# Optimization experiments

Measured on AMD Instinct MI355X. Metric: run time of the kernel, lower is better.

Reference implementation:

```python
import jax, jax.numpy as jnp
import numpy as np

N, E, D, H, C, ED = 50000, 800000, 128, 4, 32, 1
EFF = H * C  # 128 == D, so residual proj is Identity
FFN_H = 2 * EFF


def setup_inputs() -> dict:
    key = jax.random.key(0)
    ks = jax.random.split(key, 16)
    def p(k, shape, fan_in):
        return jax.random.normal(k, shape, dtype=jnp.float32) / np.sqrt(fan_in)
    return {
        "x": jax.random.normal(ks[0], (N, D), dtype=jnp.float32),
        "edge_attr": jax.random.normal(ks[1], (E, ED), dtype=jnp.float32),
        "W_l": p(ks[2], (D, EFF), D),
        "b_l": jnp.zeros((EFF,), jnp.float32),
        "W_r": p(ks[3], (D, EFF), D),
        "b_r": jnp.zeros((EFF,), jnp.float32),
        "W_e": p(ks[4], (ED, EFF), ED),
        "att": p(ks[5], (H, C), C),
        "bias_out": jnp.zeros((EFF,), jnp.float32),
        "W_gate": p(ks[6], (EFF, 1), EFF),
        "b_gate": jnp.zeros((1,), jnp.float32),
        "W_ffn1": p(ks[7], (EFF, FFN_H), EFF),
        "b_ffn1": jnp.zeros((FFN_H,), jnp.float32),
        "W_ffn2": p(ks[8], (FFN_H, EFF), FFN_H),
        "b_ffn2": jnp.zeros((EFF,), jnp.float32),
        "ln_gamma": jnp.ones((EFF,), jnp.float32),
        "ln_beta": jnp.zeros((EFF,), jnp.float32),
        "edge_index": jax.random.randint(ks[9], (2, E), 0, N, dtype=jnp.int32),
    }


def _gat_block(x, edge_attr, W_l, b_l, W_r, b_r, W_e, att, bias_out,
               W_gate, b_gate, W_ffn1, b_ffn1, W_ffn2, b_ffn2,
               ln_gamma, ln_beta, edge_index):
    n = x.shape[0]
    # add self loops (PyG default), edge_attr filled with mean
    loop = jnp.arange(n, dtype=edge_index.dtype)
    src = jnp.concatenate([edge_index[0], loop])
    dst = jnp.concatenate([edge_index[1], loop])
    ea = jnp.concatenate([edge_attr,
                          jnp.broadcast_to(edge_attr.mean(0, keepdims=True), (n, edge_attr.shape[1]))])
    # GATv2: separate source/target transforms + edge embedding
    xl = (x @ W_l + b_l).reshape(n, H, C)   # source features
    xr = (x @ W_r + b_r).reshape(n, H, C)   # target features
    ee = (ea @ W_e).reshape(-1, H, C)
    xj = xl[src]                             # [Et,H,C]
    m = jax.nn.leaky_relu(xj + xr[dst] + ee, negative_slope=0.2)
    logits = jnp.einsum('ehc,hc->eh', m, att)           # [Et,H]
    # segment softmax over destination nodes
    mx = jax.ops.segment_max(logits, dst, num_segments=n)
    ex = jnp.exp(logits - mx[dst])
    den = jax.ops.segment_sum(ex, dst, num_segments=n)
    alpha = ex / den[dst]
    out = jax.ops.segment_sum(xj * alpha[..., None], dst, num_segments=n)
    out = out.reshape(n, EFF) + bias_out
    # block: ELU, gated residual (proj is Identity since D==EFF), FFN, LayerNorm
    h = jax.nn.elu(out)
    gate = jax.nn.sigmoid(h @ W_gate + b_gate)
    y = gate * h + (1.0 - gate) * x
    ffn = jax.nn.relu(y @ W_ffn1 + b_ffn1) @ W_ffn2 + b_ffn2
    y = y + ffn
    mu = y.mean(-1, keepdims=True)
    var = y.var(-1, keepdims=True)
    y = (y - mu) * jax.lax.rsqrt(var + 1e-5) * ln_gamma + ln_beta
    return y  # dropout is identity in eval mode


def reference(x, edge_attr, W_l, b_l, W_r, b_r, W_e, att, bias_out,
              W_gate, b_gate, W_ffn1, b_ffn1, W_ffn2, b_ffn2,
              ln_gamma, ln_beta, edge_index):
    return _gat_block(x, edge_attr, W_l, b_l, W_r, b_r, W_e, att, bias_out,
                      W_gate, b_gate, W_ffn1, b_ffn1, W_ffn2, b_ffn2,
                      ln_gamma, ln_beta, edge_index)
```

## Files before the change

kernel.cpp:

```cpp
#include <hip/hip_runtime.h>
#include <hip/hip_bf16.h>

#define NODES 50000
#define NEDGE 800000
#define ETOT  850000

#define SCHUNK 1024
#define SBLK   ((NODES + SCHUNK - 1) / SCHUNK)

#define XF_TILES 1563
#define PREP_BLKS 1024
#define FUSE_GRID 2587

typedef __hip_bfloat16 bf16;
typedef __attribute__((ext_vector_type(8))) short bf16x8;
typedef __attribute__((ext_vector_type(4))) float f32x4;

__device__ __forceinline__ bf16 f2bf(float v) { return __float2bfloat16(v); }
__device__ __forceinline__ float bflo(unsigned int v) { return __uint_as_float(v << 16); }
__device__ __forceinline__ float bfhi(unsigned int v) { return __uint_as_float(v & 0xffff0000u); }

__device__ __forceinline__ unsigned int pack2(float a, float b) {
    bf16 x = f2bf(a), y = f2bf(b);
    unsigned short xs = *reinterpret_cast<unsigned short*>(&x);
    unsigned short ys = *reinterpret_cast<unsigned short*>(&y);
    return ((unsigned int)ys << 16) | (unsigned int)xs;
}

__device__ __forceinline__ unsigned short bfbits(float v) {
    bf16 x = f2bf(v);
    return *reinterpret_cast<unsigned short*>(&x);
}

__device__ __forceinline__ void split8(const float* v, bf16x8& hi, bf16x8& lo) {
    #pragma unroll
    for (int e = 0; e < 8; ++e) {
        unsigned short hb = bfbits(v[e]);
        float hv = __uint_as_float((unsigned int)hb << 16);
        unsigned short lb = bfbits(v[e] - hv);
        ((short*)&hi)[e] = (short)hb;
        ((short*)&lo)[e] = (short)lb;
    }
}

__global__ __launch_bounds__(256) void k_wxf(const float* W_l, const float* W_r,
                                             bf16* wlh, bf16* wll,
                                             bf16* wrh, bf16* wrl) {
    int tid = blockIdx.x * blockDim.x + threadIdx.x;
    int m = tid >> 14;
    int t = tid & 16383;
    int c = t >> 7, k = t & 127;
    const float* W = m ? W_r : W_l;
    float v = W[k * 128 + c];
    unsigned short hb = bfbits(v);
    float hv = __uint_as_float((unsigned int)hb << 16);
    bf16* dh = m ? wrh : wlh;
    bf16* dl = m ? wrl : wll;
    dh[t] = f2bf(v);
    dl[t] = f2bf(v - hv);
}

__global__ __launch_bounds__(256) void k_fuse(const float* edge_attr, const int* ei,
                                              float* sum_ea, int* cnt,
                                              unsigned char* tmp_rank,
                                              const float* x,
                                              const bf16* wlh, const bf16* wll,
                                              const bf16* wrh, const bf16* wrl,
                                              const float* b_l, const float* b_r,
                                              bf16* xl, bf16* xr) {
    __shared__ __align__(16) float s_x[32][132];
    const int bid = blockIdx.x;
    int idx;
    bool isprep;
    if (bid < 2 * PREP_BLKS) { isprep = (bid & 1); idx = bid >> 1; }
    else { isprep = false; idx = PREP_BLKS + (bid - 2 * PREP_BLKS); }

    if (isprep) {
        int tid = idx * 256 + threadIdx.x;
        const int stride = PREP_BLKS * 256;
        float local = 0.f;
        for (int e = tid; e < ETOT; e += stride) {
            int dst = (e < NEDGE) ? ei[NEDGE + e] : (e - NEDGE);
            int r = atomicAdd(&cnt[dst], 1);
            tmp_rank[e] = (unsigned char)r;
            if (e < NEDGE) local += edge_attr[e];
        }
        #pragma unroll
        for (int s = 1; s < 64; s <<= 1) local += __shfl_xor(local, s, 64);
        if ((threadIdx.x & 63) == 0) atomicAdd(sum_ea, local);
        return;
    }

    const int tid = threadIdx.x;
    const int n0 = idx * 32;
    for (int it = 0; it < 4; ++it) {
        int idx4 = (it * 256 + tid) * 4;
        int n = idx4 >> 7, j = idx4 & 127;
        int node = n0 + n;
        float4 v = make_float4(0.f, 0.f, 0.f, 0.f);
        if (node < NODES) v = *(const float4*)(x + node * 128 + j);
        *(float4*)&s_x[n][j] = v;
    }
    __syncthreads();

    const int wv4  = tid >> 6;
    const int ln   = tid & 63;
    const int lrow = ln & 15;
    const int lk8  = (ln >> 4) << 3;
    const int m    = wv4 >> 1;
    const int cb   = (wv4 & 1) * 64;
    const bf16* Bh = m ? wrh : wlh;
    const bf16* Bl = m ? wrl : wll;
    const float* bias = m ? b_r : b_l;

    f32x4 acc[2][4];
    #pragma unroll
    for (int mt = 0; mt < 2; ++mt)
        #pragma unroll
        for (int i = 0; i < 4; ++i)
            acc[mt][i] = (f32x4){0.f, 0.f, 0.f, 0.f};
    #pragma unroll
    for (int kk = 0; kk < 4; ++kk) {
        int k0 = kk * 32 + lk8;
        float a0f[8], a1f[8];
        *(float4*)&a0f[0] = *(const float4*)&s_x[lrow][k0];
        *(float4*)&a0f[4] = *(const float4*)&s_x[lrow][k0 + 4];
        *(float4*)&a1f[0] = *(const float4*)&s_x[16 + lrow][k0];
        *(float4*)&a1f[4] = *(const float4*)&s_x[16 + lrow][k0 + 4];
        bf16x8 a0h, a0l, a1h, a1l;
        split8(a0f, a0h, a0l);
        split8(a1f, a1h, a1l);
        #pragma unroll
        for (int i = 0; i < 4; ++i) {
            int col = cb + (i << 4) + lrow;
            bf16x8 bh = *(const bf16x8*)(Bh + col * 128 + k0);
            bf16x8 bl = *(const bf16x8*)(Bl + col * 128 + k0);
            acc[0][i] = __builtin_amdgcn_mfma_f32_16x16x32_bf16(a0l, bh, acc[0][i], 0, 0, 0);
            acc[0][i] = __builtin_amdgcn_mfma_f32_16x16x32_bf16(a0h, bl, acc[0][i], 0, 0, 0);
            acc[0][i] = __builtin_amdgcn_mfma_f32_16x16x32_bf16(a0h, bh, acc[0][i], 0, 0, 0);
            acc[1][i] = __builtin_amdgcn_mfma_f32_16x16x32_bf16(a1l, bh, acc[1][i], 0, 0, 0);
            acc[1][i] = __builtin_amdgcn_mfma_f32_16x16x32_bf16(a1h, bl, acc[1][i], 0, 0, 0);
            acc[1][i] = __builtin_amdgcn_mfma_f32_16x16x32_bf16(a1h, bh, acc[1][i], 0, 0, 0);
        }
    }
    __syncthreads();
    bf16* s_o = (bf16*)&s_x[0][0];
    #pragma unroll
    for (int mt = 0; mt < 2; ++mt) {
        #pragma unroll
        for (int i = 0; i < 4; ++i) {
            int colg = cb + (i << 4) + lrow;
            float bv = bias[colg];
            #pragma unroll
            for (int r = 0; r < 4; ++r) {
                int row = (mt << 4) + ((ln >> 4) << 2) + r;
                s_o[row * 264 + m * 136 + colg] = f2bf(acc[mt][i][r] + bv);
            }
        }
    }
    __syncthreads();
    #pragma unroll
    for (int rep = 0; rep < 2; ++rep) {
        int idx2 = rep * 256 + tid;
        int row = idx2 >> 4, cc = (idx2 & 15) * 8;
        int node = n0 + row;
        if (node < NODES) {
            *(float4*)(xl + node * 128 + cc) = *(const float4*)(s_o + row * 264 + cc);
            *(float4*)(xr + node * 128 + cc) = *(const float4*)(s_o + row * 264 + 136 + cc);
        }
    }
}

__global__ __launch_bounds__(256) void k_scan1(const int* count, int* bsum) {
    __shared__ int s_w[4];
    const int t = threadIdx.x, b = blockIdx.x;
    const int base = b * SCHUNK + t * 4;
    int s = 0;
    #pragma unroll
    for (int e = 0; e < 4; ++e) {
        int i = base + e;
        if (i < NODES) s += count[i];
    }
    #pragma unroll
    for (int d = 1; d < 64; d <<= 1) s += __shfl_xor(s, d, 64);
    if ((t & 63) == 0) s_w[t >> 6] = s;
    __syncthreads();
    if (t == 0) bsum[b] = s_w[0] + s_w[1] + s_w[2] + s_w[3];
}

__global__ __launch_bounds__(256) void k_scan3(const int* count, const int* bsum,
                                               int* off) {
    __shared__ int s_w[4];
    __shared__ int s_base;
    const int t = threadIdx.x, b = blockIdx.x;
    const int lane = t & 63, wv = t >> 6;
    if (t < 64) {
        int v = (t < b) ? bsum[t] : 0;
        #pragma unroll
        for (int d = 1; d < 64; d <<= 1) v += __shfl_xor(v, d, 64);
        if (t == 0) s_base = v;
    }
    const int base = b * SCHUNK + t * 4;
    int v[4];
    int s = 0;
    #pragma unroll
    for (int e = 0; e < 4; ++e) {
        int i = base + e;
        v[e] = (i < NODES) ? count[i] : 0;
        s += v[e];
    }
    int inc = s;
    #pragma unroll
    for (int d = 1; d < 64; d <<= 1) {
        int y = __shfl_up(inc, d, 64);
        if (lane >= d) inc += y;
    }
    if (lane == 63) s_w[wv] = inc;
    __syncthreads();
    int woff = 0;
    #pragma unroll
    for (int w = 0; w < 4; ++w) if (w < wv) woff += s_w[w];
    int run = s_base + woff + (inc - s);
    #pragma unroll
    for (int e = 0; e < 4; ++e) {
        int i = base + e;
        if (i < NODES) {
            off[i] = run; run += v[e];
            if (i == NODES - 1) off[NODES] = run;
        }
    }
}

__global__ __launch_bounds__(256) void k_wconv(const float* W1, const float* W2,
                                               bf16* w1h, bf16* w1l,
                                               bf16* w2h, bf16* w2l) {
    int tid = blockIdx.x * blockDim.x + threadIdx.x;
    if (tid < 32768) {
        int c = tid >> 7, k = tid & 127;
        float v = W1[k * 256 + c];
        unsigned short hb = bfbits(v);
        float hv = __uint_as_float((unsigned int)hb << 16);
        w1h[tid] = f2bf(v);
        w1l[tid] = f2bf(v - hv);
    } else {
        int t = tid - 32768;
        int c = t >> 8, k = t & 255;
        float v = W2[k * 128 + c];
        unsigned short hb = bfbits(v);
        float hv = __uint_as_float((unsigned int)hb << 16);
        w2h[t] = f2bf(v);
        w2l[t] = f2bf(v - hv);
    }
}

__global__ __launch_bounds__(256) void k_place(const int* ei, const float* edge_attr,
                                               const float* sum_ea, const int* off,
                                               const unsigned char* tmp_rank,
                                               unsigned int* perm) {
    const float meanv = sum_ea[0] * (1.f / (float)NEDGE);
    int tid = blockIdx.x * blockDim.x + threadIdx.x;
    int stride = gridDim.x * blockDim.x;
    for (int e = tid; e < ETOT; e += stride) {
        int src, dst; float eav;
        if (e < NEDGE) { src = ei[e]; dst = ei[NEDGE + e]; eav = edge_attr[e]; }
        else           { src = e - NEDGE; dst = src; eav = meanv; }
        int pos = off[dst] + (int)tmp_rank[e];
        perm[pos] = ((unsigned int)bfbits(eav) << 16) | (unsigned int)src;
    }
}

__global__ __launch_bounds__(256) void k_agg(const unsigned int* xl32,
                                             const unsigned int* xr32,
                                             const unsigned int* perm, const int* off,
                                             const float* W_e, const float* att,
                                             float* outp) {
    const int lane = threadIdx.x & 63;
    const int wave0 = blockIdx.x * 4 + (threadIdx.x >> 6);
    const int nwaves = gridDim.x * 4;
    const int c = 2 * lane;
    const float we1 = W_e[c], we2 = W_e[c + 1];
    const float a1 = att[c], a2 = att[c + 1];
    for (int n = wave0; n < NODES; n += nwaves) {
        unsigned int xru = xr32[n * 64 + lane];
        float xr1 = bflo(xru), xr2 = bfhi(xru);
        int s0 = off[n], s1 = off[n + 1];
        float m = -1e30f, l = 0.f, acc1 = 0.f, acc2 = 0.f;
        int j = s0;
        for (; j + 4 <= s1; j += 4) {
            unsigned int u0 = perm[j];
            unsigned int u1 = perm[j + 1];
            unsigned int u2 = perm[j + 2];
            unsigned int u3 = perm[j + 3];
            unsigned int g0 = xl32[(u0 & 0xffffu) * 64 + lane];
            unsigned int g1 = xl32[(u1 & 0xffffu) * 64 + lane];
            unsigned int g2 = xl32[(u2 & 0xffffu) * 64 + lane];
            unsigned int g3 = xl32[(u3 & 0xffffu) * 64 + lane];
            float e0 = bfhi(u0), e1 = bfhi(u1), e2 = bfhi(u2), e3 = bfhi(u3);
            float x01 = bflo(g0), x02 = bfhi(g0);
            float x11 = bflo(g1), x12 = bfhi(g1);
            float x21 = bflo(g2), x22 = bfhi(g2);
            float x31 = bflo(g3), x32 = bfhi(g3);
            float p0, p1, p2, p3;
            {
                float v1 = x01 + xr1 + e0 * we1, v2 = x02 + xr2 + e0 * we2;
                v1 = (v1 > 0.f) ? v1 : 0.2f * v1;
                v2 = (v2 > 0.f) ? v2 : 0.2f * v2;
                p0 = v1 * a1 + v2 * a2;
            }
            {
                float v1 = x11 + xr1 + e1 * we1, v2 = x12 + xr2 + e1 * we2;
                v1 = (v1 > 0.f) ? v1 : 0.2f * v1;
                v2 = (v2 > 0.f) ? v2 : 0.2f * v2;
                p1 = v1 * a1 + v2 * a2;
            }
            {
                float v1 = x21 + xr1 + e2 * we1, v2 = x22 + xr2 + e2 * we2;
                v1 = (v1 > 0.f) ? v1 : 0.2f * v1;
                v2 = (v2 > 0.f) ? v2 : 0.2f * v2;
                p2 = v1 * a1 + v2 * a2;
            }
            {
                float v1 = x31 + xr1 + e3 * we1, v2 = x32 + xr2 + e3 * we2;
                v1 = (v1 > 0.f) ? v1 : 0.2f * v1;
                v2 = (v2 > 0.f) ? v2 : 0.2f * v2;
                p3 = v1 * a1 + v2 * a2;
            }
            p0 += __shfl_xor(p0, 1, 64); p1 += __shfl_xor(p1, 1, 64);
            p2 += __shfl_xor(p2, 1, 64); p3 += __shfl_xor(p3, 1, 64);
            p0 += __shfl_xor(p0, 2, 64); p1 += __shfl_xor(p1, 2, 64);
            p2 += __shfl_xor(p2, 2, 64); p3 += __shfl_xor(p3, 2, 64);
            p0 += __shfl_xor(p0, 4, 64); p1 += __shfl_xor(p1, 4, 64);
            p2 += __shfl_xor(p2, 4, 64); p3 += __shfl_xor(p3, 4, 64);
            p0 += __shfl_xor(p0, 8, 64); p1 += __shfl_xor(p1, 8, 64);
            p2 += __shfl_xor(p2, 8, 64); p3 += __shfl_xor(p3, 8, 64);
            float nm = fmaxf(fmaxf(m, fmaxf(p0, p1)), fmaxf(p2, p3));
            float sc = __expf(m - nm);
            float E0 = __expf(p0 - nm);
            float E1 = __expf(p1 - nm);
            float E2 = __expf(p2 - nm);
            float E3 = __expf(p3 - nm);
            l = l * sc + E0 + E1 + E2 + E3;
            acc1 = acc1 * sc + E0 * x01 + E1 * x11 + E2 * x21 + E3 * x31;
            acc2 = acc2 * sc + E0 * x02 + E1 * x12 + E2 * x22 + E3 * x32;
            m = nm;
        }
        for (; j < s1; ++j) {
            unsigned int u0 = perm[j];
            unsigned int g0 = xl32[(u0 & 0xffffu) * 64 + lane];
            float e0 = bfhi(u0);
            float x01 = bflo(g0), x02 = bfhi(g0);
            float v1 = x01 + xr1 + e0 * we1, v2 = x02 + xr2 + e0 * we2;
            v1 = (v1 > 0.f) ? v1 : 0.2f * v1;
            v2 = (v2 > 0.f) ? v2 : 0.2f * v2;
            float p = v1 * a1 + v2 * a2;
            p += __shfl_xor(p, 1, 64);
            p += __shfl_xor(p, 2, 64);
            p += __shfl_xor(p, 4, 64);
            p += __shfl_xor(p, 8, 64);
            float nm = fmaxf(m, p);
            float sc = __expf(m - nm);
            float ee = __expf(p - nm);
            l = l * sc + ee;
            acc1 = acc1 * sc + ee * x01;
            acc2 = acc2 * sc + ee * x02;
            m = nm;
        }
        float inv = 1.f / fmaxf(l, 1e-30f);
        *(float2*)(outp + n * 128 + c) = make_float2(acc1 * inv, acc2 * inv);
    }
}

__global__ __launch_bounds__(256) void k_epi(const float* out_agg, const float* x,
                                             const float* bias_out,
                                             const float* W_gate, const float* b_gate,
                                             const bf16* w1h, const bf16* w1l,
                                             const float* b_ffn1,
                                             const bf16* w2h, const bf16* w2l,
                                             const float* b_ffn2,
                                             const float* gamma, const float* beta,
                                             float* out) {
    __shared__ __align__(16) float s_y[32][132];
    __shared__ __align__(16) float s_t[32][260];
    __shared__ float s_g[32];
    __shared__ float s_mu[32], s_rs[32];
    const int tid = threadIdx.x;
    const int n0 = blockIdx.x * 32;
    int nn = NODES - n0; if (nn > 32) nn = 32;

    for (int it = 0; it < 4; ++it) {
        int idx4 = (it * 256 + tid) * 4;
        int n = idx4 >> 7, j = idx4 & 127;
        float4 w = make_float4(0.f, 0.f, 0.f, 0.f);
        if (n < nn) {
            float4 v  = *(const float4*)(out_agg + (n0 + n) * 128 + j);
            float4 bv = *(const float4*)(bias_out + j);
            float t0 = v.x + bv.x, t1 = v.y + bv.y;
            float t2 = v.z + bv.z, t3 = v.w + bv.w;
            w.x = (t0 > 0.f) ? t0 : (__expf(t0) - 1.f);
            w.y = (t1 > 0.f) ? t1 : (__expf(t1) - 1.f);
            w.z = (t2 > 0.f) ? t2 : (__expf(t2) - 1.f);
            w.w = (t3 > 0.f) ? t3 : (__expf(t3) - 1.f);
        }
        *(float4*)&s_y[n][j] = w;
    }
    __syncthreads();
    {
        int n = tid >> 3, kb = (tid & 7) * 16;
        float g = 0.f;
        #pragma unroll
        for (int k = 0; k < 16; k += 4) {
            float4 w = *(const float4*)(W_gate + kb + k);
            float4 h = *(const float4*)&s_y[n][kb + k];
            g += h.x * w.x + h.y * w.y + h.z * w.z + h.w * w.w;
        }
        g += __shfl_xor(g, 1, 64);
        g += __shfl_xor(g, 2, 64);
        g += __shfl_xor(g, 4, 64);
        if ((tid & 7) == 0) s_g[n] = 1.f / (1.f + __expf(-(g + b_gate[0])));
    }
    __syncthreads();
    for (int it = 0; it < 4; ++it) {
        int idx4 = (it * 256 + tid) * 4;
        int n = idx4 >> 7, j = idx4 & 127;
        if (n < nn) {
            float g = s_g[n];
            float4 xv = *(const float4*)(x + (n0 + n) * 128 + j);
            float4 h = *(float4*)&s_y[n][j];
            h.x = g * h.x + (1.f - g) * xv.x;
            h.y = g * h.y + (1.f - g) * xv.y;
            h.z = g * h.z + (1.f - g) * xv.z;
            h.w = g * h.w + (1.f - g) * xv.w;
            *(float4*)&s_y[n][j] = h;
        }
    }
    __syncthreads();

    const int wv   = tid >> 6;
    const int ln   = tid & 63;
    const int lrow = ln & 15;
    const int lk8  = (ln >> 4) << 3;

    f32x4 acc1[2][4];
    #pragma unroll
    for (int mt = 0; mt < 2; ++mt)
        #pragma unroll
        for (int i = 0; i < 4; ++i)
            acc1[mt][i] = (f32x4){0.f, 0.f, 0.f, 0.f};
    #pragma unroll
    for (int kk = 0; kk < 4; ++kk) {
        int k0 = kk * 32 + lk8;
        float a0f[8], a1f[8];
        *(float4*)&a0f[0] = *(const float4*)&s_y[lrow][k0];
        *(float4*)&a0f[4] = *(const float4*)&s_y[lrow][k0 + 4];
        *(float4*)&a1f[0] = *(const float4*)&s_y[16 + lrow][k0];
        *(float4*)&a1f[4] = *(const float4*)&s_y[16 + lrow][k0 + 4];
        bf16x8 a0h, a0l, a1h, a1l;
        split8(a0f, a0h, a0l);
        split8(a1f, a1h, a1l);
        #pragma unroll
        for (int i = 0; i < 4; ++i) {
            int col = (wv << 6) + (i << 4) + lrow;
            bf16x8 bh = *(const bf16x8*)(w1h + col * 128 + k0);
            bf16x8 bl = *(const bf16x8*)(w1l + col * 128 + k0);
            acc1[0][i] = __builtin_amdgcn_mfma_f32_16x16x32_bf16(a0l, bh, acc1[0][i], 0, 0, 0);
            acc1[0][i] = __builtin_amdgcn_mfma_f32_16x16x32_bf16(a0h, bl, acc1[0][i], 0, 0, 0);
            acc1[0][i] = __builtin_amdgcn_mfma_f32_16x16x32_bf16(a0h, bh, acc1[0][i], 0, 0, 0);
            acc1[1][i] = __builtin_amdgcn_mfma_f32_16x16x32_bf16(a1l, bh, acc1[1][i], 0, 0, 0);
            acc1[1][i] = __builtin_amdgcn_mfma_f32_16x16x32_bf16(a1h, bl, acc1[1][i], 0, 0, 0);
            acc1[1][i] = __builtin_amdgcn_mfma_f32_16x16x32_bf16(a1h, bh, acc1[1][i], 0, 0, 0);
        }
    }
    #pragma unroll
    for (int mt = 0; mt < 2; ++mt) {
        #pragma unroll
        for (int i = 0; i < 4; ++i) {
            int col = (wv << 6) + (i << 4) + lrow;
            float bv = b_ffn1[col];
            #pragma unroll
            for (int r = 0; r < 4; ++r) {
                int row = (mt << 4) + ((ln >> 4) << 2) + r;
                s_t[row][col] = fmaxf(acc1[mt][i][r] + bv, 0.f);
            }
        }
    }
    __syncthreads();

    f32x4 acc2[2][2];
    #pragma unroll
    for (int mt = 0; mt < 2; ++mt)
        #pragma unroll
        for (int c = 0; c < 2; ++c)
            acc2[mt][c] = (f32x4){0.f, 0.f, 0.f, 0.f};
    #pragma unroll
    for (int kk = 0; kk < 8; ++kk) {
        int k0 = kk * 32 + lk8;
        float a0f[8], a1f[8];
        *(float4*)&a0f[0] = *(const float4*)&s_t[lrow][k0];
        *(float4*)&a0f[4] = *(const float4*)&s_t[lrow][k0 + 4];
        *(float4*)&a1f[0] = *(const float4*)&s_t[16 + lrow][k0];
        *(float4*)&a1f[4] = *(const float4*)&s_t[16 + lrow][k0 + 4];
        bf16x8 a0h, a0l, a1h, a1l;
        split8(a0f, a0h, a0l);
        split8(a1f, a1h, a1l);
        #pragma unroll
        for (int c = 0; c < 2; ++c) {
            int col = (wv << 5) + (c << 4) + lrow;
            bf16x8 bh = *(const bf16x8*)(w2h + col * 256 + k0);
            bf16x8 bl = *(const bf16x8*)(w2l + col * 256 + k0);
            acc2[0][c] = __builtin_amdgcn_mfma_f32_16x16x32_bf16(a0l, bh, acc2[0][c], 0, 0, 0);
            acc2[0][c] = __builtin_amdgcn_mfma_f32_16x16x32_bf16(a0h, bl, acc2[0][c], 0, 0, 0);
            acc2[0][c] = __builtin_amdgcn_mfma_f32_16x16x32_bf16(a0h, bh, acc2[0][c], 0, 0, 0);
            acc2[1][c] = __builtin_amdgcn_mfma_f32_16x16x32_bf16(a1l, bh, acc2[1][c], 0, 0, 0);
            acc2[1][c] = __builtin_amdgcn_mfma_f32_16x16x32_bf16(a1h, bl, acc2[1][c], 0, 0, 0);
            acc2[1][c] = __builtin_amdgcn_mfma_f32_16x16x32_bf16(a1h, bh, acc2[1][c], 0, 0, 0);
        }
    }
    #pragma unroll
    for (int mt = 0; mt < 2; ++mt) {
        #pragma unroll
        for (int c = 0; c < 2; ++c) {
            int col = (wv << 5) + (c << 4) + lrow;
            float bv = b_ffn2[col];
            #pragma unroll
            for (int r = 0; r < 4; ++r) {
                int row = (mt << 4) + ((ln >> 4) << 2) + r;
                s_y[row][col] += acc2[mt][c][r] + bv;
            }
        }
    }
    __syncthreads();
    {
        int n = tid >> 3, kb = (tid & 7) * 16;
        float s = 0.f, ss = 0.f;
        #pragma unroll
        for (int k = 0; k < 16; k += 4) {
            float4 v = *(const float4*)&s_y[n][kb + k];
            s  += v.x + v.y + v.z + v.w;
            ss += v.x * v.x + v.y * v.y + v.z * v.z + v.w * v.w;
        }
        s  += __shfl_xor(s, 1, 64);  ss += __shfl_xor(ss, 1, 64);
        s  += __shfl_xor(s, 2, 64);  ss += __shfl_xor(ss, 2, 64);
        s  += __shfl_xor(s, 4, 64);  ss += __shfl_xor(ss, 4, 64);
        if ((tid & 7) == 0) {
            float mu = s * (1.f / 128.f);
            float var = ss * (1.f / 128.f) - mu * mu;
            s_mu[n] = mu;
            s_rs[n] = rsqrtf(fmaxf(var, 0.f) + 1e-5f);
        }
    }
    __syncthreads();
    for (int it = 0; it < 4; ++it) {
        int idx4 = (it * 256 + tid) * 4;
        int n = idx4 >> 7, j = idx4 & 127;
        if (n < nn) {
            float mu = s_mu[n], rs = s_rs[n];
            float4 gv = *(const float4*)(gamma + j);
            float4 bv = *(const float4*)(beta + j);
            float4 v = *(const float4*)&s_y[n][j];
            float4 o;
            o.x = (v.x - mu) * rs * gv.x + bv.x;
            o.y = (v.y - mu) * rs * gv.y + bv.y;
            o.z = (v.z - mu) * rs * gv.z + bv.z;
            o.w = (v.w - mu) * rs * gv.w + bv.w;
            *(float4*)(out + (n0 + n) * 128 + j) = o;
        }
    }
}

extern "C" void kernel_launch(void* const* d_in, const int* in_sizes, int n_in,
                              void* d_out, int out_size, void* d_ws, size_t ws_size,
                              hipStream_t stream) {
    const float* x         = (const float*)d_in[0];
    const float* edge_attr = (const float*)d_in[1];
    const int* edge_index  = (const int*)d_in[17];
    float* out = (float*)d_out;

    char* base = (char*)d_ws;
    float* sum_ea  = (float*)(base + 16);
    int*   cnt     = (int*)  (base + 32);
    int*   off     = (int*)  (base + 200032);
    unsigned int* perm = (unsigned int*)(base + 600064);
    bf16*  xl      = (bf16*) (base + 4000064);
    bf16*  xr      = (bf16*) (base + 16800064);
    int*   bsum    = (int*)  (base + 600064);
    bf16*  wxlh    = (bf16*) (base + 600064 + 1024);
    bf16*  wxll    = (bf16*) (base + 600064 + 1024 + 32768);
    bf16*  wxrh    = (bf16*) (base + 600064 + 1024 + 65536);
    bf16*  wxrl    = (bf16*) (base + 600064 + 1024 + 98304);
    bf16*  w1t_hi  = (bf16*) (base + 32);
    bf16*  w1t_lo  = (bf16*) (base + 32 + 65536);
    bf16*  w2t_hi  = (bf16*) (base + 400064);
    bf16*  w2t_lo  = (bf16*) (base + 400064 + 65536);
    unsigned char* tmp_rank = (unsigned char*)d_out;

    hipMemsetAsync(sum_ea, 0, 16, stream);
    hipMemsetAsync(cnt, 0, NODES * sizeof(int), stream);

    const int NTILES = (NODES + 31) / 32;

    k_wxf   <<<128, 256, 0, stream>>>((const float*)d_in[2], (const float*)d_in[4],
                                      wxlh, wxll, wxrh, wxrl);
    k_fuse  <<<FUSE_GRID, 256, 0, stream>>>(edge_attr, edge_index, sum_ea, cnt,
                                            tmp_rank, x,
                                            wxlh, wxll, wxrh, wxrl,
                                            (const float*)d_in[3], (const float*)d_in[5],
                                            xl, xr);
    k_scan1 <<<SBLK, 256, 0, stream>>>(cnt, bsum);
    k_scan3 <<<SBLK, 256, 0, stream>>>(cnt, bsum, off);
    k_place <<<1024, 256, 0, stream>>>(edge_index, edge_attr, sum_ea, off,
                                       tmp_rank, perm);
    k_wconv <<<256, 256, 0, stream>>>((const float*)d_in[11], (const float*)d_in[13],
                                      w1t_hi, w1t_lo, w2t_hi, w2t_lo);
    k_agg   <<<3125, 256, 0, stream>>>((const unsigned int*)xl,
                                       (const unsigned int*)xr,
                                       perm, off,
                                       (const float*)d_in[6], (const float*)d_in[7],
                                       out);
    k_epi   <<<NTILES, 256, 0, stream>>>(out, x, (const float*)d_in[8],
                                         (const float*)d_in[9], (const float*)d_in[10],
                                         w1t_hi, w1t_lo, (const float*)d_in[12],
                                         w2t_hi, w2t_lo, (const float*)d_in[14],
                                         (const float*)d_in[15], (const float*)d_in[16],
                                         out);
}
```

Baseline: 350.5 us.

## Replace global-atomic counting sort with two-level LDS radix bucketing of edges

Builds the destination-sorted CSR in two levels instead of one. First, 256 blocks each count edges per coarse 1024-node range in shared memory, and a single-block scan turns those counts into per-block offsets. Edges are then scattered into range buckets, and 49 large blocks group each range by node with LDS atomics, writing off and perm. This removes 850k global atomics on per-node counters, the byte rank buffer and the memset of the counts, at the cost of an extra pass over an 8-byte temporary, a serial scan kernel and only 49 blocks in the grouping step.

```diff
diff --git a/kernel.cpp b/kernel.cpp
--- a/kernel.cpp
+++ b/kernel.cpp
@@ -5,12 +5,13 @@
 #define NEDGE 800000
 #define ETOT  850000
 
-#define SCHUNK 1024
-#define SBLK   ((NODES + SCHUNK - 1) / SCHUNK)
+#define NRANGE 49
+#define SB 256
+#define ES ((ETOT + SB - 1) / SB)
 
 #define XF_TILES 1563
-#define PREP_BLKS 1024
-#define FUSE_GRID 2587
+#define HIST_BLKS 256
+#define FUSE_GRID (2 * HIST_BLKS + (XF_TILES - HIST_BLKS))
 
 typedef __hip_bfloat16 bf16;
 typedef __attribute__((ext_vector_type(8))) short bf16x8;
@@ -61,8 +62,7 @@
 }
 
 __global__ __launch_bounds__(256) void k_fuse(const float* edge_attr, const int* ei,
-                                              float* sum_ea, int* cnt,
-                                              unsigned char* tmp_rank,
+                                              float* sum_ea, int* rhist,
                                               const float* x,
                                               const bf16* wlh, const bf16* wll,
                                               const bf16* wrh, const bf16* wrl,
@@ -72,22 +72,27 @@
     const int bid = blockIdx.x;
     int idx;
     bool isprep;
-    if (bid < 2 * PREP_BLKS) { isprep = (bid & 1); idx = bid >> 1; }
-    else { isprep = false; idx = PREP_BLKS + (bid - 2 * PREP_BLKS); }
+    if (bid < 2 * HIST_BLKS) { isprep = (bid & 1); idx = bid >> 1; }
+    else { isprep = false; idx = HIST_BLKS + (bid - 2 * HIST_BLKS); }
 
     if (isprep) {
-        int tid = idx * 256 + threadIdx.x;
-        const int stride = PREP_BLKS * 256;
+        int* hcnt = (int*)&s_x[0][0];
+        const int t = threadIdx.x;
+        if (t < 64) hcnt[t] = 0;
+        __syncthreads();
+        const int e0 = idx * ES;
+        int e1 = e0 + ES; if (e1 > ETOT) e1 = ETOT;
         float local = 0.f;
-        for (int e = tid; e < ETOT; e += stride) {
+        for (int e = e0 + t; e < e1; e += 256) {
             int dst = (e < NEDGE) ? ei[NEDGE + e] : (e - NEDGE);
-            int r = atomicAdd(&cnt[dst], 1);
-            tmp_rank[e] = (unsigned char)r;
+            atomicAdd(&hcnt[dst >> 10], 1);
             if (e < NEDGE) local += edge_attr[e];
         }
         #pragma unroll
         for (int s = 1; s < 64; s <<= 1) local += __shfl_xor(local, s, 64);
-        if ((threadIdx.x & 63) == 0) atomicAdd(sum_ea, local);
+        if ((t & 63) == 0) atomicAdd(sum_ea, local);
+        __syncthreads();
+        if (t < 64) rhist[idx * 64 + t] = hcnt[t];
         return;
     }
 
@@ -171,63 +176,91 @@
     }
 }
 
-__global__ __launch_bounds__(256) void k_scan1(const int* count, int* bsum) {
+__global__ __launch_bounds__(256) void k_rscan(int* rhist, int* base_r, int* off) {
     __shared__ int s_w[4];
-    const int t = threadIdx.x, b = blockIdx.x;
-    const int base = b * SCHUNK + t * 4;
-    int s = 0;
-    #pragma unroll
-    for (int e = 0; e < 4; ++e) {
-        int i = base + e;
-        if (i < NODES) s += count[i];
-    }
-    #pragma unroll
-    for (int d = 1; d < 64; d <<= 1) s += __shfl_xor(s, d, 64);
-    if ((t & 63) == 0) s_w[t >> 6] = s;
-    __syncthreads();
-    if (t == 0) bsum[b] = s_w[0] + s_w[1] + s_w[2] + s_w[3];
-}
-
-__global__ __launch_bounds__(256) void k_scan3(const int* count, const int* bsum,
-                                               int* off) {
-    __shared__ int s_w[4];
-    __shared__ int s_base;
-    const int t = threadIdx.x, b = blockIdx.x;
-    const int lane = t & 63, wv = t >> 6;
-    if (t < 64) {
-        int v = (t < b) ? bsum[t] : 0;
-        #pragma unroll
-        for (int d = 1; d < 64; d <<= 1) v += __shfl_xor(v, d, 64);
-        if (t == 0) s_base = v;
-    }
-    const int base = b * SCHUNK + t * 4;
-    int v[4];
-    int s = 0;
-    #pragma unroll
-    for (int e = 0; e < 4; ++e) {
-        int i = base + e;
-        v[e] = (i < NODES) ? count[i] : 0;
-        s += v[e];
-    }
-    int inc = s;
+    __shared__ int s_run;
+    const int t = threadIdx.x, lane = t & 63, w = t >> 6;
+    if (t == 0) s_run = 0;
+    __syncthreads();
+    for (int r = 0; r < NRANGE; ++r) {
+        int v = rhist[t * 64 + r];
+        int inc = v;
+        #pragma unroll
+        for (int d = 1; d < 64; d <<= 1) {
+            int y = __shfl_up(inc, d, 64);
+            if (lane >= d) inc += y;
+        }
+        if (lane == 63) s_w[w] = inc;
+        __syncthreads();
+        int woff = 0;
+        #pragma unroll
+        for (int ww = 0; ww < 4; ++ww) if (ww < w) woff += s_w[ww];
+        int tot = s_w[0] + s_w[1] + s_w[2] + s_w[3];
+        int runv = s_run;
+        rhist[t * 64 + r] = runv + woff + (inc - v);
+        if (t == 0) base_r[r] = runv;
+        __syncthreads();
+        if (t == 0) s_run = runv + tot;
+        __syncthreads();
+    }
+    if (t == 0) { base_r[NRANGE] = ETOT; off[NODES] = ETOT; }
+}
+
+__global__ __launch_bounds__(256) void k_scatter(const int* ei, const float* edge_attr,
+                                                 const float* sum_ea, const int* rhist,
+                                                 uint2* tmp2) {
+    __shared__ int cur[64];
+    const int b = blockIdx.x, t = threadIdx.x;
+    if (t < 64) cur[t] = rhist[b * 64 + t];
+    __syncthreads();
+    const float meanv = sum_ea[0] * (1.f / (float)NEDGE);
+    const int e0 = b * ES;
+    int e1 = e0 + ES; if (e1 > ETOT) e1 = ETOT;
+    for (int e = e0 + t; e < e1; e += 256) {
+        int src, dst; float eav;
+        if (e < NEDGE) { src = ei[e]; dst = ei[NEDGE + e]; eav = edge_attr[e]; }
+        else           { src = e - NEDGE; dst = src; eav = meanv; }
+        int pos = atomicAdd(&cur[dst >> 10], 1);
+        tmp2[pos] = make_uint2((unsigned int)dst,
+                               ((unsigned int)bfbits(eav) << 16) | (unsigned int)src);
+    }
+}
+
+__global__ __launch_bounds__(1024) void k_group(const uint2* tmp2, const int* base_r,
+                                                int* off, unsigned int* perm) {
+    __shared__ int lcnt[1024];
+    __shared__ int s_w16[16];
+    const int r = blockIdx.x, t = threadIdx.x;
+    const int lane = t & 63, w = t >> 6;
+    const int n0 = r << 10;
+    const int s0 = base_r[r], s1 = base_r[r + 1];
+    lcnt[t] = 0;
+    __syncthreads();
+    for (int i = s0 + t; i < s1; i += 1024) {
+        int d = (int)tmp2[i].x;
+        atomicAdd(&lcnt[d - n0], 1);
+    }
+    __syncthreads();
+    int v = lcnt[t];
+    int inc = v;
     #pragma unroll
     for (int d = 1; d < 64; d <<= 1) {
         int y = __shfl_up(inc, d, 64);
         if (lane >= d) inc += y;
     }
-    if (lane == 63) s_w[wv] = inc;
+    if (lane == 63) s_w16[w] = inc;
     __syncthreads();
     int woff = 0;
     #pragma unroll
-    for (int w = 0; w < 4; ++w) if (w < wv) woff += s_w[w];
-    int run = s_base + woff + (inc - s);
-    #pragma unroll
-    for (int e = 0; e < 4; ++e) {
-        int i = base + e;
-        if (i < NODES) {
-            off[i] = run; run += v[e];
-            if (i == NODES - 1) off[NODES] = run;
-        }
+    for (int ww = 0; ww < 16; ++ww) if (ww < w) woff += s_w16[ww];
+    int pos0 = s0 + woff + (inc - v);
+    lcnt[t] = pos0;
+    if (n0 + t < NODES) off[n0 + t] = pos0;
+    __syncthreads();
+    for (int i = s0 + t; i < s1; i += 1024) {
+        uint2 p = tmp2[i];
+        int pos = atomicAdd(&lcnt[(int)p.x - n0], 1);
+        perm[pos] = p.y;
     }
 }
 
@@ -250,22 +283,6 @@
         float hv = __uint_as_float((unsigned int)hb << 16);
         w2h[t] = f2bf(v);
         w2l[t] = f2bf(v - hv);
-    }
-}
-
-__global__ __launch_bounds__(256) void k_place(const int* ei, const float* edge_attr,
-                                               const float* sum_ea, const int* off,
-                                               const unsigned char* tmp_rank,
-                                               unsigned int* perm) {
-    const float meanv = sum_ea[0] * (1.f / (float)NEDGE);
-    int tid = blockIdx.x * blockDim.x + threadIdx.x;
-    int stride = gridDim.x * blockDim.x;
-    for (int e = tid; e < ETOT; e += stride) {
-        int src, dst; float eav;
-        if (e < NEDGE) { src = ei[e]; dst = ei[NEDGE + e]; eav = edge_attr[e]; }
-        else           { src = e - NEDGE; dst = src; eav = meanv; }
-        int pos = off[dst] + (int)tmp_rank[e];
-        perm[pos] = ((unsigned int)bfbits(eav) << 16) | (unsigned int)src;
     }
 }
 
@@ -577,49 +594,46 @@
 
     char* base = (char*)d_ws;
     float* sum_ea  = (float*)(base + 16);
-    int*   cnt     = (int*)  (base + 32);
+    int*   rhist   = (int*)  (base + 32);
+    bf16*  w1t_hi  = (bf16*) (base + 32 + 65536);
+    bf16*  w1t_lo  = (bf16*) (base + 32 + 131072);
     int*   off     = (int*)  (base + 200032);
+    int*   base_r  = (int*)  (base + 400064);
+    bf16*  w2t_hi  = (bf16*) (base + 400064 + 256);
+    bf16*  w2t_lo  = (bf16*) (base + 400064 + 256 + 65536);
     unsigned int* perm = (unsigned int*)(base + 600064);
     bf16*  xl      = (bf16*) (base + 4000064);
     bf16*  xr      = (bf16*) (base + 16800064);
-    int*   bsum    = (int*)  (base + 600064);
     bf16*  wxlh    = (bf16*) (base + 600064 + 1024);
     bf16*  wxll    = (bf16*) (base + 600064 + 1024 + 32768);
     bf16*  wxrh    = (bf16*) (base + 600064 + 1024 + 65536);
     bf16*  wxrl    = (bf16*) (base + 600064 + 1024 + 98304);
-    bf16*  w1t_hi  = (bf16*) (base + 32);
-    bf16*  w1t_lo  = (bf16*) (base + 32 + 65536);
-    bf16*  w2t_hi  = (bf16*) (base + 400064);
-    bf16*  w2t_lo  = (bf16*) (base + 400064 + 65536);
-    unsigned char* tmp_rank = (unsigned char*)d_out;
+    uint2* tmp2    = (uint2*)d_out;
 
     hipMemsetAsync(sum_ea, 0, 16, stream);
-    hipMemsetAsync(cnt, 0, NODES * sizeof(int), stream);
 
     const int NTILES = (NODES + 31) / 32;
 
-    k_wxf   <<<128, 256, 0, stream>>>((const float*)d_in[2], (const float*)d_in[4],
-                                      wxlh, wxll, wxrh, wxrl);
-    k_fuse  <<<FUSE_GRID, 256, 0, stream>>>(edge_attr, edge_index, sum_ea, cnt,
-                                            tmp_rank, x,
-                                            wxlh, wxll, wxrh, wxrl,
-                                            (const float*)d_in[3], (const float*)d_in[5],
-                                            xl, xr);
-    k_scan1 <<<SBLK, 256, 0, stream>>>(cnt, bsum);
-    k_scan3 <<<SBLK, 256, 0, stream>>>(cnt, bsum, off);
-    k_place <<<1024, 256, 0, stream>>>(edge_index, edge_attr, sum_ea, off,
-                                       tmp_rank, perm);
-    k_wconv <<<256, 256, 0, stream>>>((const float*)d_in[11], (const float*)d_in[13],
-                                      w1t_hi, w1t_lo, w2t_hi, w2t_lo);
-    k_agg   <<<3125, 256, 0, stream>>>((const unsigned int*)xl,
-                                       (const unsigned int*)xr,
-                                       perm, off,
-                                       (const float*)d_in[6], (const float*)d_in[7],
-                                       out);
-    k_epi   <<<NTILES, 256, 0, stream>>>(out, x, (const float*)d_in[8],
-                                         (const float*)d_in[9], (const float*)d_in[10],
-                                         w1t_hi, w1t_lo, (const float*)d_in[12],
-                                         w2t_hi, w2t_lo, (const float*)d_in[14],
-                                         (const float*)d_in[15], (const float*)d_in[16],
+    k_wxf     <<<128, 256, 0, stream>>>((const float*)d_in[2], (const float*)d_in[4],
+                                        wxlh, wxll, wxrh, wxrl);
+    k_fuse    <<<FUSE_GRID, 256, 0, stream>>>(edge_attr, edge_index, sum_ea, rhist,
+                                              x, wxlh, wxll, wxrh, wxrl,
+                                              (const float*)d_in[3], (const float*)d_in[5],
+                                              xl, xr);
+    k_rscan   <<<1, 256, 0, stream>>>(rhist, base_r, off);
+    k_scatter <<<SB, 256, 0, stream>>>(edge_index, edge_attr, sum_ea, rhist, tmp2);
+    k_group   <<<NRANGE, 1024, 0, stream>>>(tmp2, base_r, off, perm);
+    k_wconv   <<<256, 256, 0, stream>>>((const float*)d_in[11], (const float*)d_in[13],
+                                        w1t_hi, w1t_lo, w2t_hi, w2t_lo);
+    k_agg     <<<3125, 256, 0, stream>>>((const unsigned int*)xl,
+                                         (const unsigned int*)xr,
+                                         perm, off,
+                                         (const float*)d_in[6], (const float*)d_in[7],
                                          out);
-}
+    k_epi     <<<NTILES, 256, 0, stream>>>(out, x, (const float*)d_in[8],
+                                           (const float*)d_in[9], (const float*)d_in[10],
+                                           w1t_hi, w1t_lo, (const float*)d_in[12],
+                                           w2t_hi, w2t_lo, (const float*)d_in[14],
+                                           (const float*)d_in[15], (const float*)d_in[16],
+                                           out);
+}
```

New measurement: 349.7 us. About the same (-0.2%).
